# Kernel optimization log

Hardware: AMD Instinct MI355X
Metric: run time of the kernel (lower is better)

## Reference

```python
import jax, jax.numpy as jnp
import numpy as np

N_NODES = 50000
N_EDGES = 400000
HEADS = 3
CH = 128
NEG_SLOPE = 0.2
EPS = 1e-16


def setup_inputs() -> dict:
    key = jax.random.key(0)
    ks = jax.random.split(key, 10)
    return {
        "x": jax.random.normal(ks[0], (N_NODES, 9), jnp.float32),
        "emb_w": jax.random.normal(ks[1], (9, 128), jnp.float32) * 0.1,
        "emb_b": jax.random.normal(ks[2], (128,), jnp.float32) * 0.1,
        "gat_w": jax.random.normal(ks[3], (128, HEADS * CH), jnp.float32) * 0.05,
        "att_src": jax.random.normal(ks[4], (HEADS, CH), jnp.float32) * 0.1,
        "att_dst": jax.random.normal(ks[5], (HEADS, CH), jnp.float32) * 0.1,
        "gat_bias": jax.random.normal(ks[6], (CH,), jnp.float32) * 0.1,
        "out_w": jax.random.normal(ks[7], (128, 4), jnp.float32) * 0.1,
        "out_b": jax.random.normal(ks[8], (4,), jnp.float32) * 0.1,
        "edge_index": jax.random.randint(ks[9], (2, N_EDGES), 0, N_NODES, jnp.int64 if jax.config.jax_enable_x64 else jnp.int32),
    }


def reference(x, emb_w, emb_b, gat_w, att_src, att_dst, gat_bias, out_w, out_b, edge_index):
    n = x.shape[0]
    h = x @ emb_w + emb_b                                   # [N,128]
    # add self loops (PyG GATConv default)
    loops = jnp.arange(n, dtype=edge_index.dtype)
    src = jnp.concatenate([edge_index[0], loops])
    dst = jnp.concatenate([edge_index[1], loops])
    xh = (h @ gat_w).reshape(n, HEADS, CH)                  # [N,H,C]
    a_src = jnp.einsum('nhc,hc->nh', xh, att_src)           # [N,H]
    a_dst = jnp.einsum('nhc,hc->nh', xh, att_dst)           # [N,H]
    e = a_src[src] + a_dst[dst]                             # [E,H]
    e = jax.nn.leaky_relu(e, NEG_SLOPE)
    # segment softmax over destination node
    e_max = jax.ops.segment_max(e, dst, num_segments=n)
    e = jnp.exp(e - e_max[dst])
    denom = jax.ops.segment_sum(e, dst, num_segments=n)
    alpha = e / (denom[dst] + EPS)                          # [E,H]
    msg = xh[src] * alpha[:, :, None]                       # [E,H,C]
    agg = jax.ops.segment_sum(msg, dst, num_segments=n)     # [N,H,C]
    out = agg.mean(axis=1) + gat_bias                       # concat=False -> head mean
    x_new = out + h                                         # residual
    return x_new @ out_w + out_b                            # [N,4]
```

## Files before the change

### kernel.cpp

```cpp
#include <hip/hip_runtime.h>
#include <hip/hip_bf16.h>
#include <cstdint>

#define NEG 0.2f
#define SBS 256
#define PADK 56

typedef __attribute__((ext_vector_type(8))) short bf16x8;
typedef __attribute__((ext_vector_type(8))) unsigned short ushort8;
typedef __attribute__((ext_vector_type(4))) float f32x4;

__device__ __forceinline__ float bf2f(unsigned short u){
  return __uint_as_float(((unsigned)u)<<16);
}
__device__ __forceinline__ unsigned short f2bf(float f){
  __hip_bfloat16 b = __float2bfloat16(f);
  return *reinterpret_cast<unsigned short*>(&b);
}

__global__ __launch_bounds__(256)
void embed_kernel(const float* __restrict__ x, const float* __restrict__ emb_w,
                  const float* __restrict__ emb_b, const float* __restrict__ gat_w,
                  const float* __restrict__ att_src, const float* __restrict__ att_dst,
                  unsigned short* __restrict__ h_bf, float* __restrict__ a_s,
                  float* __restrict__ a_d, int* __restrict__ deg, int nN)
{
  __shared__ float watt[768];
  int tid = threadIdx.x;

  #pragma unroll
  for (int r=0;r<3;r++){
    int o = tid + r*256;
    int isD = (o >= 384);
    int t2 = isD ? (o-384) : o;
    int h = t2 >> 7, k = t2 & 127;
    const float* att = isD ? (att_dst + h*128) : (att_src + h*128);
    const float* gw  = gat_w + (size_t)k*384 + h*128;
    float dot = 0.f;
    #pragma unroll 8
    for (int c=0;c<128;c++) dot += gw[c]*att[c];
    watt[o] = dot;
  }
  __syncthreads();

  int n = blockIdx.x*256 + tid;
  if (n < nN) deg[n] = 0;
  if (n >= nN) return;

  float xv[9];
  #pragma unroll
  for (int k=0;k<9;k++) xv[k] = x[(size_t)n*9 + k];

  float s0=0.f,s1=0.f,s2=0.f, d0=0.f,d1=0.f,d2=0.f;
  unsigned short* hrow = h_bf + (size_t)n*128;

  #pragma unroll 4
  for (int c0=0; c0<128; c0+=8){
    unsigned short pk[8];
    #pragma unroll
    for (int j=0;j<8;j++){
      int c = c0 + j;
      float acc = emb_b[c];
      #pragma unroll
      for (int k=0;k<9;k++) acc += xv[k]*emb_w[k*128+c];
      pk[j] = f2bf(acc);
      s0 += acc*watt[c]; s1 += acc*watt[128+c]; s2 += acc*watt[256+c];
      d0 += acc*watt[384+c]; d1 += acc*watt[512+c]; d2 += acc*watt[640+c];
    }
    *(int4*)(hrow + c0) = *(int4*)pk;
  }
  a_s[(size_t)n*3+0]=s0; a_s[(size_t)n*3+1]=s1; a_s[(size_t)n*3+2]=s2;
  a_d[(size_t)n*3+0]=d0; a_d[(size_t)n*3+1]=d1; a_d[(size_t)n*3+2]=d2;
}

__global__ __launch_bounds__(256)
void deg_kernel(const int* __restrict__ ei, int* __restrict__ deg,
                const float* __restrict__ gat_w,
                unsigned short* __restrict__ Bt2, int nE, int ebN)
{
  if (blockIdx.x < (unsigned)ebN){
    int e = blockIdx.x*256 + threadIdx.x;
    if (e < nE) atomicAdd(&deg[ei[nE + e]], 1);
  } else {
    int i = (blockIdx.x - ebN)*256 + threadIdx.x;
    if (i < 12*128*32){
      int ks  = i >> 12;
      int rem = i & 4095;
      int col = rem >> 5;
      int kk  = rem & 31;
      int t = ks*32 + kk;
      int h = t >> 7, k = t & 127;
      Bt2[i] = f2bf(gat_w[(size_t)k*384 + h*128 + col] * (1.f/3.f));
    }
  }
}

__global__ __launch_bounds__(SBS)
void blocksum_kernel(const int* __restrict__ deg, int* __restrict__ bsum, int nN)
{
  int i = blockIdx.x*SBS + threadIdx.x;
  int v = (i < nN) ? deg[i]+1 : 0;
  #pragma unroll
  for (int off=32; off; off>>=1) v += __shfl_down(v, off);
  __shared__ int ws[SBS/64];
  if ((threadIdx.x&63)==0) ws[threadIdx.x>>6] = v;
  __syncthreads();
  if (threadIdx.x==0){
    int s=0;
    #pragma unroll
    for (int i2=0;i2<SBS/64;i2++) s += ws[i2];
    bsum[blockIdx.x]=s;
  }
}

__global__ __launch_bounds__(256)
void scansum_kernel(const int* __restrict__ bsum, int* __restrict__ boff, int nB)
{
  __shared__ int s[256];
  int t = threadIdx.x;
  int v = (t < nB) ? bsum[t] : 0;
  s[t] = v;
  __syncthreads();
  for (int off=1; off<256; off<<=1){
    int add = (t >= off) ? s[t-off] : 0;
    __syncthreads();
    s[t] += add;
    __syncthreads();
  }
  if (t < nB) boff[t] = (t==0) ? 0 : s[t-1];
}

__global__ __launch_bounds__(SBS)
void blockscan_kernel(const int* __restrict__ deg, const int* __restrict__ boff,
                      int* __restrict__ rowptr, int* __restrict__ cursor, int nN)
{
  __shared__ int s[SBS];
  int t = threadIdx.x;
  int i = blockIdx.x*SBS + t;
  int v = (i < nN) ? deg[i]+1 : 0;
  s[t] = v;
  __syncthreads();
  for (int off=1; off<SBS; off<<=1){
    int add = (t >= off) ? s[t-off] : 0;
    __syncthreads();
    s[t] += add;
    __syncthreads();
  }
  int excl = boff[blockIdx.x] + ((t==0) ? 0 : s[t-1]);
  if (i < nN){ rowptr[i] = excl; cursor[i] = excl; }
  if (i == nN-1) rowptr[nN] = excl + v;
}

__global__ __launch_bounds__(256)
void scatter_kernel(const int* __restrict__ ei, int* __restrict__ cursor,
                    const float* __restrict__ a_s, const float* __restrict__ a_d,
                    const int* __restrict__ rowptr, float4* __restrict__ val,
                    int nE, int ebN, int nN)
{
  if (blockIdx.x < (unsigned)ebN){
    int e = blockIdx.x*256 + threadIdx.x;
    if (e < nE){
      int s = ei[e], d = ei[nE + e];
      float e0 = a_s[(size_t)s*3+0] + a_d[(size_t)d*3+0]; e0 = e0>0.f ? e0 : NEG*e0;
      float e1 = a_s[(size_t)s*3+1] + a_d[(size_t)d*3+1]; e1 = e1>0.f ? e1 : NEG*e1;
      float e2 = a_s[(size_t)s*3+2] + a_d[(size_t)d*3+2]; e2 = e2>0.f ? e2 : NEG*e2;
      int pos = atomicAdd(&cursor[d], 1);
      val[pos] = make_float4(__expf(e0), __expf(e1), __expf(e2), __int_as_float(s));
    }
  } else {
    int n = (blockIdx.x - ebN)*256 + threadIdx.x;
    if (n < nN){
      float e0 = a_s[(size_t)n*3+0] + a_d[(size_t)n*3+0]; e0 = e0>0.f ? e0 : NEG*e0;
      float e1 = a_s[(size_t)n*3+1] + a_d[(size_t)n*3+1]; e1 = e1>0.f ? e1 : NEG*e1;
      float e2 = a_s[(size_t)n*3+2] + a_d[(size_t)n*3+2]; e2 = e2>0.f ? e2 : NEG*e2;
      val[rowptr[n+1]-1] = make_float4(__expf(e0), __expf(e1), __expf(e2),
                                       __int_as_float(n));
    }
  }
}

__global__ __launch_bounds__(256)
void gather_kernel(const int* __restrict__ rowptr, const float4* __restrict__ val,
                   const unsigned short* __restrict__ h_bf,
                   unsigned short* __restrict__ hagg, int nN)
{
  int wave = threadIdx.x >> 6, lane = threadIdx.x & 63;
  int g   = lane >> 4;
  int lin = lane & 15;
  int n = blockIdx.x*16 + wave*4 + g;
  int valid = (n < nN);
  int nc = valid ? n : (nN-1);

  int ro   = rowptr[nc];
  int degT = valid ? (rowptr[nc+1] - ro) : 0;

  float a0[8], a1[8], a2[8];
  #pragma unroll
  for (int c=0;c<8;c++){ a0[c]=0.f; a1[c]=0.f; a2[c]=0.f; }
  float den0=0.f, den1=0.f, den2=0.f;

  const unsigned short* hb = h_bf + 8*lin;
  const float4* vrow = val + ro;

  int j = 0;
  for (; j+1 < degT; j += 2){
    float4 vA = vrow[j];
    float4 vB = vrow[j+1];
    int sA = __float_as_int(vA.w);
    int sB = __float_as_int(vB.w);
    ushort8 ha = *(const ushort8*)(hb + (size_t)sA*128);
    ushort8 hc = *(const ushort8*)(hb + (size_t)sB*128);
    den0 += vA.x + vB.x; den1 += vA.y + vB.y; den2 += vA.z + vB.z;
    #pragma unroll
    for (int c=0;c<8;c++){
      float fa = bf2f(ha[c]), fb = bf2f(hc[c]);
      a0[c] += vA.x*fa + vB.x*fb;
      a1[c] += vA.y*fa + vB.y*fb;
      a2[c] += vA.z*fa + vB.z*fb;
    }
  }
  if (j < degT){
    float4 vA = vrow[j];
    int sA = __float_as_int(vA.w);
    ushort8 ha = *(const ushort8*)(hb + (size_t)sA*128);
    den0 += vA.x; den1 += vA.y; den2 += vA.z;
    #pragma unroll
    for (int c=0;c<8;c++){
      float fa = bf2f(ha[c]);
      a0[c] += vA.x*fa; a1[c] += vA.y*fa; a2[c] += vA.z*fa;
    }
  }

  if (valid){
    float w0 = 1.f/(den0+1e-16f);
    float w1 = 1.f/(den1+1e-16f);
    float w2 = 1.f/(den2+1e-16f);
    unsigned short o0[8], o1[8], o2[8];
    #pragma unroll
    for (int c=0;c<8;c++){
      o0[c] = f2bf(a0[c]*w0);
      o1[c] = f2bf(a1[c]*w1);
      o2[c] = f2bf(a2[c]*w2);
    }
    size_t bi = (size_t)n*384 + 8*lin;
    *(int4*)(hagg + bi      ) = *(int4*)o0;
    *(int4*)(hagg + bi + 128) = *(int4*)o1;
    *(int4*)(hagg + bi + 256) = *(int4*)o2;
  }
}

__global__ __launch_bounds__(256)
void gemm2_kernel(const unsigned short* __restrict__ hagg,
                  const unsigned short* __restrict__ Bt2,
                  const unsigned short* __restrict__ h_bf,
                  const float* __restrict__ gat_bias,
                  const float* __restrict__ out_w, const float* __restrict__ out_b,
                  float* __restrict__ out, int nN)
{
  __shared__ __align__(16) unsigned short Bs[2][128*PADK];
  int tid  = threadIdx.x;
  int wave = tid >> 6, lane = tid & 63;
  int cl = lane & 15, kg = lane >> 4;
  int r0 = blockIdx.x*64 + wave*16;
  int rowA = min(r0 + cl, nN-1);
  const unsigned short* aBase = hagg + (size_t)rowA*384 + kg*8;

  int scol = tid >> 1, shalf = tid & 1;
  int dstI = scol*(PADK/8) + shalf*2;

  {
    const int4* src = (const int4*)Bt2;
    int4 t0 = src[2*tid], t1 = src[2*tid+1];
    ((int4*)Bs[0])[dstI]   = t0;
    ((int4*)Bs[0])[dstI+1] = t1;
  }
  f32x4 acc[8];
  #pragma unroll
  for (int f=0;f<8;f++) acc[f] = (f32x4){0.f,0.f,0.f,0.f};
  bf16x8 aCur = *(const bf16x8*)(aBase);
  __syncthreads();

  #pragma unroll
  for (int ks=0; ks<12; ks++){
    int4 t0, t1; bf16x8 aNext;
    if (ks < 11){
      const int4* src = (const int4*)(Bt2 + (size_t)(ks+1)*4096);
      t0 = src[2*tid]; t1 = src[2*tid+1];
      aNext = *(const bf16x8*)(aBase + (ks+1)*32);
    }
    const unsigned short* bs = Bs[ks & 1];
    #pragma unroll
    for (int f=0;f<8;f++){
      bf16x8 b = *(const bf16x8*)(bs + (f*16 + cl)*PADK + kg*8);
      acc[f] = __builtin_amdgcn_mfma_f32_16x16x32_bf16(aCur, b, acc[f], 0, 0, 0);
    }
    if (ks < 11){
      int4* dst = (int4*)Bs[(ks+1) & 1];
      dst[dstI]   = t0;
      dst[dstI+1] = t1;
      aCur = aNext;
    }
    __syncthreads();
  }

  float p[4][4];
  #pragma unroll
  for (int r=0;r<4;r++)
    #pragma unroll
    for (int j=0;j<4;j++) p[r][j]=0.f;

  #pragma unroll
  for (int f=0;f<8;f++){
    int col = f*16 + cl;
    float bias = gat_bias[col];
    float w0=out_w[col*4+0], w1=out_w[col*4+1], w2=out_w[col*4+2], w3=out_w[col*4+3];
    #pragma unroll
    for (int r=0;r<4;r++){
      int row = r0 + kg*4 + r;
      float hres = (row < nN) ? bf2f(h_bf[(size_t)row*128 + col]) : 0.f;
      float xn = acc[f][r] + bias + hres;
      p[r][0] += xn*w0; p[r][1] += xn*w1; p[r][2] += xn*w2; p[r][3] += xn*w3;
    }
  }
  #pragma unroll
  for (int off=1; off<16; off<<=1){
    #pragma unroll
    for (int r=0;r<4;r++)
      #pragma unroll
      for (int j=0;j<4;j++) p[r][j] += __shfl_xor(p[r][j], off);
  }
  if (cl == 0){
    #pragma unroll
    for (int r=0;r<4;r++){
      int row = r0 + kg*4 + r;
      if (row < nN){
        float4 o = {p[r][0]+out_b[0], p[r][1]+out_b[1], p[r][2]+out_b[2], p[r][3]+out_b[3]};
        *(float4*)(out + (size_t)row*4) = o;
      }
    }
  }
}

extern "C" void kernel_launch(void* const* d_in, const int* in_sizes, int n_in,
                              void* d_out, int out_size, void* d_ws, size_t ws_size,
                              hipStream_t stream) {
  const float* x       = (const float*)d_in[0];
  const float* emb_w   = (const float*)d_in[1];
  const float* emb_b   = (const float*)d_in[2];
  const float* gat_w   = (const float*)d_in[3];
  const float* att_src = (const float*)d_in[4];
  const float* att_dst = (const float*)d_in[5];
  const float* gat_bias= (const float*)d_in[6];
  const float* out_w   = (const float*)d_in[7];
  const float* out_b   = (const float*)d_in[8];
  const int*   ei      = (const int*)d_in[9];
  float* out = (float*)d_out;

  int nN = in_sizes[0]/9;
  int nE = in_sizes[9]/2;
  int nB = (nN + SBS - 1) / SBS;
  int ebN = (nE + 255)/256;

  char* p = (char*)d_ws;
  auto alloc = [&](size_t bytes)->char*{
    char* r = p; p += (bytes + 255) & ~(size_t)255; return r;
  };
  unsigned short* h_bf   = (unsigned short*)alloc((size_t)nN*128*2);
  float*          a_s    = (float*)         alloc((size_t)nN*3*4);
  float*          a_d    = (float*)         alloc((size_t)nN*3*4);
  unsigned short* Bt2    = (unsigned short*)alloc((size_t)12*128*32*2);
  int*            deg    = (int*)           alloc((size_t)nN*4);
  int*            rowptr = (int*)           alloc(((size_t)nN+1)*4);
  int*            cursor = (int*)           alloc((size_t)nN*4);
  int*            bsum   = (int*)           alloc((size_t)nB*4);
  int*            boff   = (int*)           alloc((size_t)nB*4);
  float4*         val    = (float4*)        alloc(((size_t)nE+nN)*16);
  unsigned short* hagg   = (unsigned short*)alloc((size_t)nN*384*2);

  embed_kernel<<<nB, 256, 0, stream>>>(
      x, emb_w, emb_b, gat_w, att_src, att_dst, h_bf, a_s, a_d, deg, nN);

  deg_kernel<<<ebN + 192, 256, 0, stream>>>(ei, deg, gat_w, Bt2, nE, ebN);

  blocksum_kernel<<<nB, SBS, 0, stream>>>(deg, bsum, nN);
  scansum_kernel<<<1, 256, 0, stream>>>(bsum, boff, nB);
  blockscan_kernel<<<nB, SBS, 0, stream>>>(deg, boff, rowptr, cursor, nN);

  scatter_kernel<<<ebN + nB, 256, 0, stream>>>(
      ei, cursor, a_s, a_d, rowptr, val, nE, ebN, nN);

  gather_kernel<<<(nN+15)/16, 256, 0, stream>>>(
      rowptr, val, h_bf, hagg, nN);

  gemm2_kernel<<<(nN+63)/64, 256, 0, stream>>>(
      hagg, Bt2, h_bf, gat_bias, out_w, out_b, out, nN);
}
```

Baseline: 208.0 us.

## Fuse gather with output GEMM and replace three-pass scan with atomic allocation

The three-kernel prefix scan is replaced by a single alloc kernel. Each block scans its degrees locally and takes a base offset through an atomicAdd on a global counter, so CSR segments are no longer in node order. The gather and the second GEMM are fused: 32 aggregated rows are staged in LDS and fed straight to MFMA, with B read directly from global memory. This drops the hagg round trip and two launches, but only half the waves do the matmul and B is no longer cached in shared memory.

```diff
diff --git a/kernel.cpp b/kernel.cpp
--- a/kernel.cpp
+++ b/kernel.cpp
@@ -4,7 +4,6 @@
 
 #define NEG 0.2f
 #define SBS 256
-#define PADK 56
 
 typedef __attribute__((ext_vector_type(8))) short bf16x8;
 typedef __attribute__((ext_vector_type(8))) unsigned short ushort8;
@@ -23,7 +22,8 @@
                   const float* __restrict__ emb_b, const float* __restrict__ gat_w,
                   const float* __restrict__ att_src, const float* __restrict__ att_dst,
                   unsigned short* __restrict__ h_bf, float* __restrict__ a_s,
-                  float* __restrict__ a_d, int* __restrict__ deg, int nN)
+                  float* __restrict__ a_d, int* __restrict__ deg,
+                  int* __restrict__ gcount, int nN)
 {
   __shared__ float watt[768];
   int tid = threadIdx.x;
@@ -45,6 +45,7 @@
 
   int n = blockIdx.x*256 + tid;
   if (n < nN) deg[n] = 0;
+  if (blockIdx.x==0 && tid==0) gcount[0] = 0;
   if (n >= nN) return;
 
   float xv[9];
@@ -95,67 +96,36 @@
   }
 }
 
-__global__ __launch_bounds__(SBS)
-void blocksum_kernel(const int* __restrict__ deg, int* __restrict__ bsum, int nN)
-{
-  int i = blockIdx.x*SBS + threadIdx.x;
-  int v = (i < nN) ? deg[i]+1 : 0;
-  #pragma unroll
-  for (int off=32; off; off>>=1) v += __shfl_down(v, off);
-  __shared__ int ws[SBS/64];
-  if ((threadIdx.x&63)==0) ws[threadIdx.x>>6] = v;
+__global__ __launch_bounds__(256)
+void alloc_kernel(const int* __restrict__ deg, int* __restrict__ gcount,
+                  int* __restrict__ rowptr, int* __restrict__ cursor, int nN)
+{
+  int tid = threadIdx.x, wave = tid>>6, lane = tid&63;
+  int n = blockIdx.x*256 + tid;
+  int v = (n < nN) ? deg[n]+1 : 0;
+  int sc = v;
+  #pragma unroll
+  for (int off=1; off<64; off<<=1){
+    int t = __shfl_up(sc, off);
+    if (lane >= off) sc += t;
+  }
+  __shared__ int ws[4];
+  __shared__ int bbase;
+  if (lane==63) ws[wave] = sc;
   __syncthreads();
-  if (threadIdx.x==0){
-    int s=0;
-    #pragma unroll
-    for (int i2=0;i2<SBS/64;i2++) s += ws[i2];
-    bsum[blockIdx.x]=s;
-  }
-}
-
-__global__ __launch_bounds__(256)
-void scansum_kernel(const int* __restrict__ bsum, int* __restrict__ boff, int nB)
-{
-  __shared__ int s[256];
-  int t = threadIdx.x;
-  int v = (t < nB) ? bsum[t] : 0;
-  s[t] = v;
+  if (tid==0) bbase = atomicAdd(gcount, ws[0]+ws[1]+ws[2]+ws[3]);
   __syncthreads();
-  for (int off=1; off<256; off<<=1){
-    int add = (t >= off) ? s[t-off] : 0;
-    __syncthreads();
-    s[t] += add;
-    __syncthreads();
-  }
-  if (t < nB) boff[t] = (t==0) ? 0 : s[t-1];
-}
-
-__global__ __launch_bounds__(SBS)
-void blockscan_kernel(const int* __restrict__ deg, const int* __restrict__ boff,
-                      int* __restrict__ rowptr, int* __restrict__ cursor, int nN)
-{
-  __shared__ int s[SBS];
-  int t = threadIdx.x;
-  int i = blockIdx.x*SBS + t;
-  int v = (i < nN) ? deg[i]+1 : 0;
-  s[t] = v;
-  __syncthreads();
-  for (int off=1; off<SBS; off<<=1){
-    int add = (t >= off) ? s[t-off] : 0;
-    __syncthreads();
-    s[t] += add;
-    __syncthreads();
-  }
-  int excl = boff[blockIdx.x] + ((t==0) ? 0 : s[t-1]);
-  if (i < nN){ rowptr[i] = excl; cursor[i] = excl; }
-  if (i == nN-1) rowptr[nN] = excl + v;
+  int wbase = 0;
+  for (int i=0;i<wave;i++) wbase += ws[i];
+  int excl = bbase + wbase + sc - v;
+  if (n < nN){ rowptr[n] = excl; cursor[n] = excl; }
 }
 
 __global__ __launch_bounds__(256)
 void scatter_kernel(const int* __restrict__ ei, int* __restrict__ cursor,
                     const float* __restrict__ a_s, const float* __restrict__ a_d,
-                    const int* __restrict__ rowptr, float4* __restrict__ val,
-                    int nE, int ebN, int nN)
+                    const int* __restrict__ rowptr, const int* __restrict__ deg,
+                    float4* __restrict__ val, int nE, int ebN, int nN)
 {
   if (blockIdx.x < (unsigned)ebN){
     int e = blockIdx.x*256 + threadIdx.x;
@@ -173,142 +143,117 @@
       float e0 = a_s[(size_t)n*3+0] + a_d[(size_t)n*3+0]; e0 = e0>0.f ? e0 : NEG*e0;
       float e1 = a_s[(size_t)n*3+1] + a_d[(size_t)n*3+1]; e1 = e1>0.f ? e1 : NEG*e1;
       float e2 = a_s[(size_t)n*3+2] + a_d[(size_t)n*3+2]; e2 = e2>0.f ? e2 : NEG*e2;
-      val[rowptr[n+1]-1] = make_float4(__expf(e0), __expf(e1), __expf(e2),
-                                       __int_as_float(n));
-    }
-  }
-}
-
-__global__ __launch_bounds__(256)
-void gather_kernel(const int* __restrict__ rowptr, const float4* __restrict__ val,
-                   const unsigned short* __restrict__ h_bf,
-                   unsigned short* __restrict__ hagg, int nN)
-{
-  int wave = threadIdx.x >> 6, lane = threadIdx.x & 63;
-  int g   = lane >> 4;
-  int lin = lane & 15;
-  int n = blockIdx.x*16 + wave*4 + g;
-  int valid = (n < nN);
-  int nc = valid ? n : (nN-1);
-
-  int ro   = rowptr[nc];
-  int degT = valid ? (rowptr[nc+1] - ro) : 0;
-
-  float a0[8], a1[8], a2[8];
-  #pragma unroll
-  for (int c=0;c<8;c++){ a0[c]=0.f; a1[c]=0.f; a2[c]=0.f; }
-  float den0=0.f, den1=0.f, den2=0.f;
-
-  const unsigned short* hb = h_bf + 8*lin;
-  const float4* vrow = val + ro;
-
-  int j = 0;
-  for (; j+1 < degT; j += 2){
-    float4 vA = vrow[j];
-    float4 vB = vrow[j+1];
-    int sA = __float_as_int(vA.w);
-    int sB = __float_as_int(vB.w);
-    ushort8 ha = *(const ushort8*)(hb + (size_t)sA*128);
-    ushort8 hc = *(const ushort8*)(hb + (size_t)sB*128);
-    den0 += vA.x + vB.x; den1 += vA.y + vB.y; den2 += vA.z + vB.z;
-    #pragma unroll
-    for (int c=0;c<8;c++){
-      float fa = bf2f(ha[c]), fb = bf2f(hc[c]);
-      a0[c] += vA.x*fa + vB.x*fb;
-      a1[c] += vA.y*fa + vB.y*fb;
-      a2[c] += vA.z*fa + vB.z*fb;
-    }
-  }
-  if (j < degT){
-    float4 vA = vrow[j];
-    int sA = __float_as_int(vA.w);
-    ushort8 ha = *(const ushort8*)(hb + (size_t)sA*128);
-    den0 += vA.x; den1 += vA.y; den2 += vA.z;
-    #pragma unroll
-    for (int c=0;c<8;c++){
-      float fa = bf2f(ha[c]);
-      a0[c] += vA.x*fa; a1[c] += vA.y*fa; a2[c] += vA.z*fa;
-    }
-  }
-
-  if (valid){
-    float w0 = 1.f/(den0+1e-16f);
-    float w1 = 1.f/(den1+1e-16f);
-    float w2 = 1.f/(den2+1e-16f);
-    unsigned short o0[8], o1[8], o2[8];
-    #pragma unroll
-    for (int c=0;c<8;c++){
-      o0[c] = f2bf(a0[c]*w0);
-      o1[c] = f2bf(a1[c]*w1);
-      o2[c] = f2bf(a2[c]*w2);
-    }
-    size_t bi = (size_t)n*384 + 8*lin;
-    *(int4*)(hagg + bi      ) = *(int4*)o0;
-    *(int4*)(hagg + bi + 128) = *(int4*)o1;
-    *(int4*)(hagg + bi + 256) = *(int4*)o2;
-  }
-}
-
-__global__ __launch_bounds__(256)
-void gemm2_kernel(const unsigned short* __restrict__ hagg,
-                  const unsigned short* __restrict__ Bt2,
-                  const unsigned short* __restrict__ h_bf,
-                  const float* __restrict__ gat_bias,
-                  const float* __restrict__ out_w, const float* __restrict__ out_b,
-                  float* __restrict__ out, int nN)
-{
-  __shared__ __align__(16) unsigned short Bs[2][128*PADK];
-  int tid  = threadIdx.x;
+      val[rowptr[n] + deg[n]] = make_float4(__expf(e0), __expf(e1), __expf(e2),
+                                            __int_as_float(n));
+    }
+  }
+}
+
+__global__ __launch_bounds__(256)
+void gathermm_kernel(const int* __restrict__ rowptr, const int* __restrict__ deg,
+                     const float4* __restrict__ val,
+                     const unsigned short* __restrict__ h_bf,
+                     const unsigned short* __restrict__ Bt2,
+                     const float* __restrict__ gat_bias,
+                     const float* __restrict__ out_w, const float* __restrict__ out_b,
+                     float* __restrict__ out, int nN)
+{
+  __shared__ __align__(16) unsigned short hs[32][392];
+  int tid = threadIdx.x;
   int wave = tid >> 6, lane = tid & 63;
+  int g = lane >> 4, lin = lane & 15;
+  int nb0 = blockIdx.x*32;
+
+  for (int pass=0; pass<2; ++pass){
+    int local = pass*16 + wave*4 + g;
+    int n = nb0 + local;
+    int valid = (n < nN);
+    int nc = valid ? n : 0;
+    int ro   = rowptr[nc];
+    int degT = valid ? (deg[nc] + 1) : 0;
+
+    float a0[8], a1[8], a2[8];
+    #pragma unroll
+    for (int c=0;c<8;c++){ a0[c]=0.f; a1[c]=0.f; a2[c]=0.f; }
+    float den0=0.f, den1=0.f, den2=0.f;
+
+    const unsigned short* hb = h_bf + 8*lin;
+    const float4* vrow = val + ro;
+
+    int j = 0;
+    for (; j+1 < degT; j += 2){
+      float4 vA = vrow[j];
+      float4 vB = vrow[j+1];
+      int sA = __float_as_int(vA.w);
+      int sB = __float_as_int(vB.w);
+      ushort8 ha = *(const ushort8*)(hb + (size_t)sA*128);
+      ushort8 hc = *(const ushort8*)(hb + (size_t)sB*128);
+      den0 += vA.x + vB.x; den1 += vA.y + vB.y; den2 += vA.z + vB.z;
+      #pragma unroll
+      for (int c=0;c<8;c++){
+        float fa = bf2f(ha[c]), fb = bf2f(hc[c]);
+        a0[c] += vA.x*fa + vB.x*fb;
+        a1[c] += vA.y*fa + vB.y*fb;
+        a2[c] += vA.z*fa + vB.z*fb;
+      }
+    }
+    if (j < degT){
+      float4 vA = vrow[j];
+      int sA = __float_as_int(vA.w);
+      ushort8 ha = *(const ushort8*)(hb + (size_t)sA*128);
+      den0 += vA.x; den1 += vA.y; den2 += vA.z;
+      #pragma unroll
+      for (int c=0;c<8;c++){
+        float fa = bf2f(ha[c]);
+        a0[c] += vA.x*fa; a1[c] += vA.y*fa; a2[c] += vA.z*fa;
+      }
+    }
+
+    if (valid){
+      float w0 = 1.f/(den0+1e-16f);
+      float w1 = 1.f/(den1+1e-16f);
+      float w2 = 1.f/(den2+1e-16f);
+      unsigned short o0[8], o1[8], o2[8];
+      #pragma unroll
+      for (int c=0;c<8;c++){
+        o0[c] = f2bf(a0[c]*w0);
+        o1[c] = f2bf(a1[c]*w1);
+        o2[c] = f2bf(a2[c]*w2);
+      }
+      unsigned short* hp = &hs[local][8*lin];
+      *(int4*)(hp      ) = *(int4*)o0;
+      *(int4*)(hp + 128) = *(int4*)o1;
+      *(int4*)(hp + 256) = *(int4*)o2;
+    }
+  }
+  __syncthreads();
+
+  if (wave >= 2) return;
   int cl = lane & 15, kg = lane >> 4;
-  int r0 = blockIdx.x*64 + wave*16;
-  int rowA = min(r0 + cl, nN-1);
-  const unsigned short* aBase = hagg + (size_t)rowA*384 + kg*8;
-
-  int scol = tid >> 1, shalf = tid & 1;
-  int dstI = scol*(PADK/8) + shalf*2;
-
-  {
-    const int4* src = (const int4*)Bt2;
-    int4 t0 = src[2*tid], t1 = src[2*tid+1];
-    ((int4*)Bs[0])[dstI]   = t0;
-    ((int4*)Bs[0])[dstI+1] = t1;
-  }
+  int rlocal = wave*16 + cl;
+  const unsigned short* aBase = &hs[rlocal][0];
+
   f32x4 acc[8];
   #pragma unroll
   for (int f=0;f<8;f++) acc[f] = (f32x4){0.f,0.f,0.f,0.f};
-  bf16x8 aCur = *(const bf16x8*)(aBase);
-  __syncthreads();
 
   #pragma unroll
   for (int ks=0; ks<12; ks++){
-    int4 t0, t1; bf16x8 aNext;
-    if (ks < 11){
-      const int4* src = (const int4*)(Bt2 + (size_t)(ks+1)*4096);
-      t0 = src[2*tid]; t1 = src[2*tid+1];
-      aNext = *(const bf16x8*)(aBase + (ks+1)*32);
-    }
-    const unsigned short* bs = Bs[ks & 1];
+    bf16x8 a = *(const bf16x8*)(aBase + ks*32 + kg*8);
     #pragma unroll
     for (int f=0;f<8;f++){
-      bf16x8 b = *(const bf16x8*)(bs + (f*16 + cl)*PADK + kg*8);
-      acc[f] = __builtin_amdgcn_mfma_f32_16x16x32_bf16(aCur, b, acc[f], 0, 0, 0);
-    }
-    if (ks < 11){
-      int4* dst = (int4*)Bs[(ks+1) & 1];
-      dst[dstI]   = t0;
-      dst[dstI+1] = t1;
-      aCur = aNext;
-    }
-    __syncthreads();
+      bf16x8 b = *(const bf16x8*)(Bt2 + (size_t)ks*4096 + (f*16 + cl)*32 + kg*8);
+      acc[f] = __builtin_amdgcn_mfma_f32_16x16x32_bf16(a, b, acc[f], 0, 0, 0);
+    }
   }
 
   float p[4][4];
   #pragma unroll
   for (int r=0;r<4;r++)
     #pragma unroll
-    for (int j=0;j<4;j++) p[r][j]=0.f;
-
+    for (int j2=0;j2<4;j2++) p[r][j2]=0.f;
+
+  int r0 = nb0 + wave*16;
   #pragma unroll
   for (int f=0;f<8;f++){
     int col = f*16 + cl;
@@ -327,7 +272,7 @@
     #pragma unroll
     for (int r=0;r<4;r++)
       #pragma unroll
-      for (int j=0;j<4;j++) p[r][j] += __shfl_xor(p[r][j], off);
+      for (int j2=0;j2<4;j2++) p[r][j2] += __shfl_xor(p[r][j2], off);
   }
   if (cl == 0){
     #pragma unroll
@@ -370,28 +315,21 @@
   float*          a_d    = (float*)         alloc((size_t)nN*3*4);
   unsigned short* Bt2    = (unsigned short*)alloc((size_t)12*128*32*2);
   int*            deg    = (int*)           alloc((size_t)nN*4);
-  int*            rowptr = (int*)           alloc(((size_t)nN+1)*4);
+  int*            rowptr = (int*)           alloc((size_t)nN*4);
   int*            cursor = (int*)           alloc((size_t)nN*4);
-  int*            bsum   = (int*)           alloc((size_t)nB*4);
-  int*            boff   = (int*)           alloc((size_t)nB*4);
+  int*            gcount = (int*)           alloc(256);
   float4*         val    = (float4*)        alloc(((size_t)nE+nN)*16);
-  unsigned short* hagg   = (unsigned short*)alloc((size_t)nN*384*2);
 
   embed_kernel<<<nB, 256, 0, stream>>>(
-      x, emb_w, emb_b, gat_w, att_src, att_dst, h_bf, a_s, a_d, deg, nN);
+      x, emb_w, emb_b, gat_w, att_src, att_dst, h_bf, a_s, a_d, deg, gcount, nN);
 
   deg_kernel<<<ebN + 192, 256, 0, stream>>>(ei, deg, gat_w, Bt2, nE, ebN);
 
-  blocksum_kernel<<<nB, SBS, 0, stream>>>(deg, bsum, nN);
-  scansum_kernel<<<1, 256, 0, stream>>>(bsum, boff, nB);
-  blockscan_kernel<<<nB, SBS, 0, stream>>>(deg, boff, rowptr, cursor, nN);
+  alloc_kernel<<<nB, 256, 0, stream>>>(deg, gcount, rowptr, cursor, nN);
 
   scatter_kernel<<<ebN + nB, 256, 0, stream>>>(
-      ei, cursor, a_s, a_d, rowptr, val, nE, ebN, nN);
-
-  gather_kernel<<<(nN+15)/16, 256, 0, stream>>>(
-      rowptr, val, h_bf, hagg, nN);
-
-  gemm2_kernel<<<(nN+63)/64, 256, 0, stream>>>(
-      hagg, Bt2, h_bf, gat_bias, out_w, out_b, out, nN);
-}
+      ei, cursor, a_s, a_d, rowptr, deg, val, nE, ebN, nN);
+
+  gathermm_kernel<<<(nN+31)/32, 256, 0, stream>>>(
+      rowptr, deg, val, h_bf, Bt2, gat_bias, out_w, out_b, out, nN);
+}
```

New measurement: 212.8 us. +2.3%, slower.
